# Performance work log

Measured on AMD Instinct MI355X. Metric: run time of the kernel, lower is better.

The kernel has to match this reference:

```python
import jax, jax.numpy as jnp
import numpy as np

B, S, E_DIM, H_DIM, WID, HGT = 64, 128, 256, 128, 64, 64


def setup_inputs() -> dict:
    key = jax.random.key(0)
    k1, k2, k3, k4 = jax.random.split(key, 4)
    e = jax.random.normal(k1, (B, S, E_DIM), dtype=jnp.float32)
    h = jax.random.normal(k2, (B, H_DIM, WID, HGT), dtype=jnp.float32)
    W = jax.random.normal(k3, (H_DIM, E_DIM), dtype=jnp.float32) * (1.0 / np.sqrt(E_DIM))
    b = jax.random.normal(k4, (H_DIM,), dtype=jnp.float32) * 0.01
    return {"e": e, "h": h, "W": W, "b": b}


def reference(e, h, W, b):
    # Linear: (B, S, e_dim) -> (B, S, h_dim)
    ep = jnp.einsum('bse,de->bsd', e, W) + b
    batch, ch, width, height = h.shape
    hv = h.reshape(batch, ch, width * height)          # (B, D, N)
    # scores s = bmm(e^T_proj, h): (B, S, N)
    s = jnp.einsum('bsd,bdn->bsn', ep, hv)
    # softmax over seq dim (dim=1 in torch)
    beta = jax.nn.softmax(s, axis=1)
    # c = sum_s e[b,d,s] * beta[b,s,n]  -> (B, D, N)  (true batched GEMM)
    c = jnp.einsum('bsd,bsn->bdn', ep, beta)
    return c.reshape(batch, ch, width, height)
```

## Files before the change

kernel.cpp:

```cpp
#include <hip/hip_runtime.h>
#include <math.h>

#define B_ 64
#define S_ 128
#define E_ 256
#define D_ 128
#define N_ 4096

typedef _Float16 f16;
typedef _Float16 f16x8 __attribute__((ext_vector_type(8)));
typedef float f32x4 __attribute__((ext_vector_type(4)));

__device__ __forceinline__ unsigned pack2(f16 a, f16 b) {
    union { f16 h[2]; unsigned u; } x;
    x.h[0] = a; x.h[1] = b; return x.u;
}

__device__ __forceinline__ f32x4 mfma16(f16x8 a, f16x8 b, f32x4 c) {
    return __builtin_amdgcn_mfma_f32_16x16x32_f16(a, b, c, 0, 0, 0);
}

__global__ __launch_bounds__(256) void k1_ep(
    const float* __restrict__ e, const float* __restrict__ W,
    const float* __restrict__ bias,
    unsigned* __restrict__ epA_h, unsigned* __restrict__ epA_l,
    unsigned* __restrict__ epT_h)
{
    __shared__ __align__(16) float el[64 * 68];
    __shared__ __align__(16) float Wl[32 * 68];
    const int t = threadIdx.x;
    const int b  = blockIdx.x >> 3;
    const int d0 = ((blockIdx.x >> 1) & 3) << 5;
    const int s0 = (blockIdx.x & 1) << 6;
    const int p = t & 15;
    const int q = t >> 4;

    float acc[2][2][2];
#pragma unroll
    for (int m = 0; m < 2; ++m)
#pragma unroll
        for (int u = 0; u < 2; ++u)
            acc[m][u][0] = acc[m][u][1] = 0.f;

    for (int kc = 0; kc < E_; kc += 64) {
#pragma unroll
        for (int it = 0; it < 4; ++it) {
            const int lin = it * 256 + t;
            const int r = lin >> 4, c4 = (lin & 15) << 2;
            *(float4*)(el + r * 68 + c4) =
                *(const float4*)(e + (b * S_ + s0 + r) * E_ + kc + c4);
        }
#pragma unroll
        for (int it = 0; it < 2; ++it) {
            const int lin = it * 256 + t;
            const int r = lin >> 4, c4 = (lin & 15) << 2;
            *(float4*)(Wl + r * 68 + c4) =
                *(const float4*)(W + (d0 + r) * E_ + kc + c4);
        }
        __syncthreads();
#pragma unroll 4
        for (int kk = 0; kk < 64; kk += 4) {
            const float4 w0 = *(const float4*)(Wl + (2 * p) * 68 + kk);
            const float4 w1 = *(const float4*)(Wl + (2 * p + 1) * 68 + kk);
#pragma unroll
            for (int u = 0; u < 2; ++u) {
                const float4 e0 = *(const float4*)(el + (2 * q + 32 * u) * 68 + kk);
                const float4 e1 = *(const float4*)(el + (2 * q + 1 + 32 * u) * 68 + kk);
                acc[0][u][0] += w0.x * e0.x + w0.y * e0.y + w0.z * e0.z + w0.w * e0.w;
                acc[0][u][1] += w0.x * e1.x + w0.y * e1.y + w0.z * e1.z + w0.w * e1.w;
                acc[1][u][0] += w1.x * e0.x + w1.y * e0.y + w1.z * e0.z + w1.w * e0.w;
                acc[1][u][1] += w1.x * e1.x + w1.y * e1.y + w1.z * e1.z + w1.w * e1.w;
            }
        }
        __syncthreads();
    }

    const float bz[2] = { bias[d0 + 2 * p], bias[d0 + 2 * p + 1] };
    f16 hi[2][2][2], lo[2][2][2];
#pragma unroll
    for (int m = 0; m < 2; ++m)
#pragma unroll
        for (int u = 0; u < 2; ++u)
#pragma unroll
            for (int v = 0; v < 2; ++v) {
                const float val = acc[m][u][v] + bz[m];
                const f16 h_ = (f16)val;
                hi[m][u][v] = h_;
                lo[m][u][v] = (f16)(val - (float)h_);
            }
#pragma unroll
    for (int u = 0; u < 2; ++u)
#pragma unroll
        for (int v = 0; v < 2; ++v) {
            const int s = s0 + 2 * q + v + 32 * u;
            const int w = (b * S_ + s) * 64 + (d0 >> 1) + p;
            epA_h[w] = pack2(hi[0][u][v], hi[1][u][v]);
            epA_l[w] = pack2(lo[0][u][v], lo[1][u][v]);
        }
#pragma unroll
    for (int m = 0; m < 2; ++m)
#pragma unroll
        for (int u = 0; u < 2; ++u) {
            const int d = d0 + 2 * p + m;
            const int w = (b * D_ + d) * 64 + (s0 >> 1) + q + 16 * u;
            epT_h[w] = pack2(hi[m][u][0], hi[m][u][1]);
        }
}

__global__ __launch_bounds__(256) void k2_attn(
    const float* __restrict__ h, const f16* __restrict__ epA_h,
    const f16* __restrict__ epA_l, const f16* __restrict__ epT_h,
    float* __restrict__ out)
{
    __shared__ __align__(16) unsigned char reg1[34816];
    __shared__ __align__(16) unsigned char reg2[17408];
    __shared__ float red1[4][64];
    __shared__ float red2[4][64];

    f16*   hT_h = (f16*)reg1;
    f16*   hT_l = (f16*)(reg1 + 17408);
    float* sc   = (float*)reg1;
    float* cb   = (float*)reg1;
    f16*   bT   = (f16*)reg2;
    float* stg  = (float*)reg2;

    const int t = threadIdx.x;
    const int b  = blockIdx.x >> 6;
    const int n0 = (blockIdx.x & 63) << 6;
    const int wid = t >> 6, lane = t & 63;
    const int l16 = lane & 15, quad = lane >> 4;

    const int jj = t & 63;
    const int dg = (t >> 6) << 3;
    unsigned* dstH = (unsigned*)hT_h;
    unsigned* dstL = (unsigned*)hT_l;
    for (int ch = 0; ch < 4; ++ch) {
#pragma unroll
        for (int r = 0; r < 2; ++r) {
            const int lin = r * 256 + t;
            const int dd = lin >> 4, m4 = (lin & 15) << 2;
            *(float4*)(stg + dd * 68 + m4) =
                *(const float4*)(h + (b * D_ + ch * 32 + dd) * N_ + n0 + m4);
        }
        __syncthreads();
        f16 vh[8], vl[8];
#pragma unroll
        for (int x = 0; x < 8; ++x) {
            const float v = stg[(dg + x) * 68 + jj];
            vh[x] = (f16)v;
            vl[x] = (f16)(v - (float)vh[x]);
        }
        const int base = jj * 68 + (ch << 4) + (dg >> 1);
#pragma unroll
        for (int y = 0; y < 4; ++y) {
            dstH[base + y] = pack2(vh[2 * y], vh[2 * y + 1]);
            dstL[base + y] = pack2(vl[2 * y], vl[2 * y + 1]);
        }
        __syncthreads();
    }

    const int sb = wid << 5;
    f32x4 acc[2][4];
#pragma unroll
    for (int mt = 0; mt < 2; ++mt)
#pragma unroll
        for (int nt = 0; nt < 4; ++nt) acc[mt][nt] = (f32x4)0.f;

    const f16* Ah = epA_h + (b * S_ + sb + l16) * D_ + quad * 8;
    const f16* Al = epA_l + (b * S_ + sb + l16) * D_ + quad * 8;
#pragma unroll
    for (int kk = 0; kk < 4; ++kk) {
        const int dc = kk << 5;
        f16x8 bh[4], bl[4];
#pragma unroll
        for (int nt = 0; nt < 4; ++nt) {
            const int idx = ((nt << 4) + l16) * 136 + dc + quad * 8;
            bh[nt] = *(const f16x8*)(hT_h + idx);
            bl[nt] = *(const f16x8*)(hT_l + idx);
        }
#pragma unroll
        for (int mt = 0; mt < 2; ++mt) {
            const f16x8 ah = *(const f16x8*)(Ah + mt * 16 * D_ + dc);
            const f16x8 al = *(const f16x8*)(Al + mt * 16 * D_ + dc);
#pragma unroll
            for (int nt = 0; nt < 4; ++nt) {
                acc[mt][nt] = mfma16(ah, bh[nt], acc[mt][nt]);
                acc[mt][nt] = mfma16(ah, bl[nt], acc[mt][nt]);
                acc[mt][nt] = mfma16(al, bh[nt], acc[mt][nt]);
            }
        }
    }
    __syncthreads();
#pragma unroll
    for (int mt = 0; mt < 2; ++mt)
#pragma unroll
        for (int nt = 0; nt < 4; ++nt)
#pragma unroll
            for (int r = 0; r < 4; ++r)
                sc[(sb + mt * 16 + quad * 4 + r) * 68 + (nt << 4) + l16] =
                    acc[mt][nt][r];
    __syncthreads();

    const int pj = t & 63, pp = t >> 6;
    float ev[32];
    float mx = -1e30f;
#pragma unroll
    for (int ss = 0; ss < 32; ++ss) {
        ev[ss] = sc[(pp * 32 + ss) * 68 + pj];
        mx = fmaxf(mx, ev[ss]);
    }
    red1[pp][pj] = mx;
    __syncthreads();
    mx = fmaxf(fmaxf(red1[0][pj], red1[1][pj]),
               fmaxf(red1[2][pj], red1[3][pj]));
    float sm = 0.f;
#pragma unroll
    for (int ss = 0; ss < 32; ++ss) {
        ev[ss] = expf(ev[ss] - mx);
        sm += ev[ss];
    }
    red2[pp][pj] = sm;
    __syncthreads();
    sm = red2[0][pj] + red2[1][pj] + red2[2][pj] + red2[3][pj];
    const float inv = 1.f / sm;
    unsigned* bTw = (unsigned*)bT;
    const int bbase = pj * 68 + pp * 16;
#pragma unroll
    for (int k = 0; k < 16; ++k)
        bTw[bbase + k] = pack2((f16)(ev[2 * k] * inv), (f16)(ev[2 * k + 1] * inv));
    __syncthreads();

    const int db = wid << 5;
    f32x4 a2[2][4];
#pragma unroll
    for (int mt = 0; mt < 2; ++mt)
#pragma unroll
        for (int nt = 0; nt < 4; ++nt) a2[mt][nt] = (f32x4)0.f;

    const f16* At = epT_h + (b * D_ + db + l16) * S_ + quad * 8;
#pragma unroll
    for (int kk = 0; kk < 4; ++kk) {
        const int scb = kk << 5;
        f16x8 bb[4];
#pragma unroll
        for (int nt = 0; nt < 4; ++nt)
            bb[nt] = *(const f16x8*)(bT + ((nt << 4) + l16) * 136 + scb + quad * 8);
#pragma unroll
        for (int mt = 0; mt < 2; ++mt) {
            const f16x8 av = *(const f16x8*)(At + mt * 16 * S_ + scb);
#pragma unroll
            for (int nt = 0; nt < 4; ++nt)
                a2[mt][nt] = mfma16(av, bb[nt], a2[mt][nt]);
        }
    }
#pragma unroll
    for (int mt = 0; mt < 2; ++mt)
#pragma unroll
        for (int nt = 0; nt < 4; ++nt)
#pragma unroll
            for (int r = 0; r < 4; ++r)
                cb[(db + mt * 16 + quad * 4 + r) * 68 + (nt << 4) + l16] =
                    a2[mt][nt][r];
    __syncthreads();

#pragma unroll
    for (int r = 0; r < 8; ++r) {
        const int lin = r * 256 + t;
        const int row = lin >> 4, c4 = (lin & 15) << 2;
        *(float4*)(out + (b * D_ + row) * N_ + n0 + c4) =
            *(float4*)(cb + row * 68 + c4);
    }
}

extern "C" void kernel_launch(void* const* d_in, const int* in_sizes, int n_in,
                              void* d_out, int out_size, void* d_ws, size_t ws_size,
                              hipStream_t stream) {
    const float* e    = (const float*)d_in[0];
    const float* h    = (const float*)d_in[1];
    const float* W    = (const float*)d_in[2];
    const float* bias = (const float*)d_in[3];
    float* out = (float*)d_out;

    unsigned* epA_h = (unsigned*)d_ws;
    unsigned* epA_l = epA_h + (B_ * S_ * D_ / 2);
    unsigned* epT_h = epA_l + (B_ * S_ * D_ / 2);

    hipLaunchKernelGGL(k1_ep, dim3(B_ * 8), dim3(256), 0, stream,
                       e, W, bias, epA_h, epA_l, epT_h);
    hipLaunchKernelGGL(k2_attn, dim3(B_ * 64), dim3(256), 0, stream,
                       h, (const f16*)epA_h, (const f16*)epA_l,
                       (const f16*)epT_h, out);
}
```

Baseline: 299.8 us.

## Halve N-tile to 32 columns, do softmax in registers, swizzle LDS, store output directly

The attention kernel now processes 32 spatial columns per block instead of 64, doubling the grid and shrinking LDS use so more blocks fit per CU. It loads the whole h tile in one pass and writes the hi/lo fp16 split into XOR-swizzled LDS. The softmax max and sum are computed on the MFMA accumulators with cross-lane shuffles plus a small LDS reduction, which removes the score round-trip through LDS. The output is written straight from registers. The epA operands are now re-read from global memory twice as often, and the direct output stores are narrower and less coalesced than the previous float4 staging.

```diff
diff --git a/kernel.cpp b/kernel.cpp
--- a/kernel.cpp
+++ b/kernel.cpp
@@ -112,164 +112,173 @@
     const f16* __restrict__ epA_l, const f16* __restrict__ epT_h,
     float* __restrict__ out)
 {
-    __shared__ __align__(16) unsigned char reg1[34816];
-    __shared__ __align__(16) unsigned char reg2[17408];
-    __shared__ float red1[4][64];
-    __shared__ float red2[4][64];
-
-    f16*   hT_h = (f16*)reg1;
-    f16*   hT_l = (f16*)(reg1 + 17408);
-    float* sc   = (float*)reg1;
-    float* cb   = (float*)reg1;
-    f16*   bT   = (f16*)reg2;
-    float* stg  = (float*)reg2;
+    __shared__ __align__(16) unsigned char regA[16384];
+    __shared__ __align__(16) unsigned char regB[18432];
+
+    f16*   hTh  = (f16*)regA;
+    f16*   hTl  = (f16*)(regA + 8192);
+    float* stg  = (float*)regB;
+    f16*   bT   = (f16*)regB;
+    float* red1 = (float*)(regB + 8704);
+    float* red2 = (float*)(regB + 9216);
 
     const int t = threadIdx.x;
-    const int b  = blockIdx.x >> 6;
-    const int n0 = (blockIdx.x & 63) << 6;
+    const int b  = blockIdx.x >> 7;
+    const int n0 = (blockIdx.x & 127) << 5;
     const int wid = t >> 6, lane = t & 63;
     const int l16 = lane & 15, quad = lane >> 4;
 
-    const int jj = t & 63;
-    const int dg = (t >> 6) << 3;
-    unsigned* dstH = (unsigned*)hT_h;
-    unsigned* dstL = (unsigned*)hT_l;
-    for (int ch = 0; ch < 4; ++ch) {
-#pragma unroll
-        for (int r = 0; r < 2; ++r) {
-            const int lin = r * 256 + t;
-            const int dd = lin >> 4, m4 = (lin & 15) << 2;
-            *(float4*)(stg + dd * 68 + m4) =
-                *(const float4*)(h + (b * D_ + ch * 32 + dd) * N_ + n0 + m4);
-        }
-        __syncthreads();
-        f16 vh[8], vl[8];
-#pragma unroll
-        for (int x = 0; x < 8; ++x) {
-            const float v = stg[(dg + x) * 68 + jj];
-            vh[x] = (f16)v;
-            vl[x] = (f16)(v - (float)vh[x]);
-        }
-        const int base = jj * 68 + (ch << 4) + (dg >> 1);
-#pragma unroll
-        for (int y = 0; y < 4; ++y) {
-            dstH[base + y] = pack2(vh[2 * y], vh[2 * y + 1]);
-            dstL[base + y] = pack2(vl[2 * y], vl[2 * y + 1]);
-        }
-        __syncthreads();
-    }
+    float4 v[4];
+#pragma unroll
+    for (int i = 0; i < 4; ++i) {
+        const int lin = i * 256 + t;
+        const int d = lin >> 3, c4 = (lin & 7) << 2;
+        v[i] = *(const float4*)(h + (b * D_ + d) * N_ + n0 + c4);
+    }
+#pragma unroll
+    for (int i = 0; i < 4; ++i) {
+        const int lin = i * 256 + t;
+        const int d = lin >> 3, c4 = (lin & 7) << 2;
+        *(float4*)(stg + d * 36 + c4) = v[i];
+    }
+    __syncthreads();
+
+    {
+        const int n = t & 31, dgrp = t >> 5;
+        f16x8 h0, h1, l0, l1;
+#pragma unroll
+        for (int x = 0; x < 16; ++x) {
+            const float val = stg[(dgrp * 16 + x) * 36 + n];
+            const f16 hi_ = (f16)val;
+            const f16 lo_ = (f16)(val - (float)hi_);
+            if (x < 8) { h0[x] = hi_; l0[x] = lo_; }
+            else       { h1[x - 8] = hi_; l1[x - 8] = lo_; }
+        }
+        const int base = n * 256 + dgrp * 32;
+        const int swz  = (n & 7) << 4;
+        *(f16x8*)((char*)hTh + ((base)      ^ swz)) = h0;
+        *(f16x8*)((char*)hTh + ((base + 16) ^ swz)) = h1;
+        *(f16x8*)((char*)hTl + ((base)      ^ swz)) = l0;
+        *(f16x8*)((char*)hTl + ((base + 16) ^ swz)) = l1;
+    }
+    __syncthreads();
 
     const int sb = wid << 5;
-    f32x4 acc[2][4];
+    f32x4 acc[2][2];
 #pragma unroll
     for (int mt = 0; mt < 2; ++mt)
 #pragma unroll
-        for (int nt = 0; nt < 4; ++nt) acc[mt][nt] = (f32x4)0.f;
+        for (int nt = 0; nt < 2; ++nt) acc[mt][nt] = (f32x4)0.f;
 
     const f16* Ah = epA_h + (b * S_ + sb + l16) * D_ + quad * 8;
     const f16* Al = epA_l + (b * S_ + sb + l16) * D_ + quad * 8;
 #pragma unroll
     for (int kk = 0; kk < 4; ++kk) {
         const int dc = kk << 5;
-        f16x8 bh[4], bl[4];
-#pragma unroll
-        for (int nt = 0; nt < 4; ++nt) {
-            const int idx = ((nt << 4) + l16) * 136 + dc + quad * 8;
-            bh[nt] = *(const f16x8*)(hT_h + idx);
-            bl[nt] = *(const f16x8*)(hT_l + idx);
+        f16x8 bh[2], bl[2];
+#pragma unroll
+        for (int nt = 0; nt < 2; ++nt) {
+            const int n = (nt << 4) + l16;
+            const int off = (n * 256 + dc * 2 + quad * 16) ^ ((n & 7) << 4);
+            bh[nt] = *(const f16x8*)((const char*)hTh + off);
+            bl[nt] = *(const f16x8*)((const char*)hTl + off);
         }
 #pragma unroll
         for (int mt = 0; mt < 2; ++mt) {
             const f16x8 ah = *(const f16x8*)(Ah + mt * 16 * D_ + dc);
             const f16x8 al = *(const f16x8*)(Al + mt * 16 * D_ + dc);
 #pragma unroll
-            for (int nt = 0; nt < 4; ++nt) {
+            for (int nt = 0; nt < 2; ++nt) {
                 acc[mt][nt] = mfma16(ah, bh[nt], acc[mt][nt]);
                 acc[mt][nt] = mfma16(ah, bl[nt], acc[mt][nt]);
                 acc[mt][nt] = mfma16(al, bh[nt], acc[mt][nt]);
             }
         }
     }
-    __syncthreads();
+
+#pragma unroll
+    for (int nt = 0; nt < 2; ++nt) {
+        float pm = -1e30f;
+#pragma unroll
+        for (int mt = 0; mt < 2; ++mt)
+#pragma unroll
+            for (int r = 0; r < 4; ++r) pm = fmaxf(pm, acc[mt][nt][r]);
+        pm = fmaxf(pm, __shfl_xor(pm, 16));
+        pm = fmaxf(pm, __shfl_xor(pm, 32));
+        if (quad == 0) red1[(((nt << 4) + l16) << 2) + wid] = pm;
+    }
+    __syncthreads();
+
+    float ev[2][2][4];
+#pragma unroll
+    for (int nt = 0; nt < 2; ++nt) {
+        const f32x4 m4 = *(const f32x4*)(red1 + (((nt << 4) + l16) << 2));
+        const float mx = fmaxf(fmaxf(m4[0], m4[1]), fmaxf(m4[2], m4[3]));
+        float ps = 0.f;
+#pragma unroll
+        for (int mt = 0; mt < 2; ++mt)
+#pragma unroll
+            for (int r = 0; r < 4; ++r) {
+                const float e_ = __expf(acc[mt][nt][r] - mx);
+                ev[mt][nt][r] = e_;
+                ps += e_;
+            }
+        ps += __shfl_xor(ps, 16);
+        ps += __shfl_xor(ps, 32);
+        if (quad == 0) red2[(((nt << 4) + l16) << 2) + wid] = ps;
+    }
+    __syncthreads();
+
+    unsigned* bTw = (unsigned*)bT;
+#pragma unroll
+    for (int nt = 0; nt < 2; ++nt) {
+        const int n = (nt << 4) + l16;
+        const f32x4 s4 = *(const f32x4*)(red2 + (n << 2));
+        const float inv = 1.f / (s4[0] + s4[1] + s4[2] + s4[3]);
+#pragma unroll
+        for (int mt = 0; mt < 2; ++mt) {
+            const int wbase = n * 68 + ((sb + mt * 16) >> 1) + quad * 2;
+            bTw[wbase]     = pack2((f16)(ev[mt][nt][0] * inv),
+                                   (f16)(ev[mt][nt][1] * inv));
+            bTw[wbase + 1] = pack2((f16)(ev[mt][nt][2] * inv),
+                                   (f16)(ev[mt][nt][3] * inv));
+        }
+    }
+    __syncthreads();
+
+    const int db = wid << 5;
+    f32x4 a2[2][2];
 #pragma unroll
     for (int mt = 0; mt < 2; ++mt)
 #pragma unroll
-        for (int nt = 0; nt < 4; ++nt)
-#pragma unroll
-            for (int r = 0; r < 4; ++r)
-                sc[(sb + mt * 16 + quad * 4 + r) * 68 + (nt << 4) + l16] =
-                    acc[mt][nt][r];
-    __syncthreads();
-
-    const int pj = t & 63, pp = t >> 6;
-    float ev[32];
-    float mx = -1e30f;
-#pragma unroll
-    for (int ss = 0; ss < 32; ++ss) {
-        ev[ss] = sc[(pp * 32 + ss) * 68 + pj];
-        mx = fmaxf(mx, ev[ss]);
-    }
-    red1[pp][pj] = mx;
-    __syncthreads();
-    mx = fmaxf(fmaxf(red1[0][pj], red1[1][pj]),
-               fmaxf(red1[2][pj], red1[3][pj]));
-    float sm = 0.f;
-#pragma unroll
-    for (int ss = 0; ss < 32; ++ss) {
-        ev[ss] = expf(ev[ss] - mx);
-        sm += ev[ss];
-    }
-    red2[pp][pj] = sm;
-    __syncthreads();
-    sm = red2[0][pj] + red2[1][pj] + red2[2][pj] + red2[3][pj];
-    const float inv = 1.f / sm;
-    unsigned* bTw = (unsigned*)bT;
-    const int bbase = pj * 68 + pp * 16;
-#pragma unroll
-    for (int k = 0; k < 16; ++k)
-        bTw[bbase + k] = pack2((f16)(ev[2 * k] * inv), (f16)(ev[2 * k + 1] * inv));
-    __syncthreads();
-
-    const int db = wid << 5;
-    f32x4 a2[2][4];
-#pragma unroll
-    for (int mt = 0; mt < 2; ++mt)
-#pragma unroll
-        for (int nt = 0; nt < 4; ++nt) a2[mt][nt] = (f32x4)0.f;
+        for (int nt = 0; nt < 2; ++nt) a2[mt][nt] = (f32x4)0.f;
 
     const f16* At = epT_h + (b * D_ + db + l16) * S_ + quad * 8;
 #pragma unroll
     for (int kk = 0; kk < 4; ++kk) {
         const int scb = kk << 5;
-        f16x8 bb[4];
-#pragma unroll
-        for (int nt = 0; nt < 4; ++nt)
+        f16x8 bb[2];
+#pragma unroll
+        for (int nt = 0; nt < 2; ++nt)
             bb[nt] = *(const f16x8*)(bT + ((nt << 4) + l16) * 136 + scb + quad * 8);
 #pragma unroll
         for (int mt = 0; mt < 2; ++mt) {
             const f16x8 av = *(const f16x8*)(At + mt * 16 * S_ + scb);
 #pragma unroll
-            for (int nt = 0; nt < 4; ++nt)
+            for (int nt = 0; nt < 2; ++nt)
                 a2[mt][nt] = mfma16(av, bb[nt], a2[mt][nt]);
         }
     }
+
+    float* ob = out + (b * D_ + db) * N_ + n0;
 #pragma unroll
     for (int mt = 0; mt < 2; ++mt)
 #pragma unroll
-        for (int nt = 0; nt < 4; ++nt)
+        for (int nt = 0; nt < 2; ++nt)
 #pragma unroll
             for (int r = 0; r < 4; ++r)
-                cb[(db + mt * 16 + quad * 4 + r) * 68 + (nt << 4) + l16] =
+                ob[(mt * 16 + quad * 4 + r) * N_ + (nt << 4) + l16] =
                     a2[mt][nt][r];
-    __syncthreads();
-
-#pragma unroll
-    for (int r = 0; r < 8; ++r) {
-        const int lin = r * 256 + t;
-        const int row = lin >> 4, c4 = (lin & 15) << 2;
-        *(float4*)(out + (b * D_ + row) * N_ + n0 + c4) =
-            *(float4*)(cb + row * 68 + c4);
-    }
 }
 
 extern "C" void kernel_launch(void* const* d_in, const int* in_sizes, int n_in,
@@ -287,7 +296,7 @@
 
     hipLaunchKernelGGL(k1_ep, dim3(B_ * 8), dim3(256), 0, stream,
                        e, W, bias, epA_h, epA_l, epT_h);
-    hipLaunchKernelGGL(k2_attn, dim3(B_ * 64), dim3(256), 0, stream,
+    hipLaunchKernelGGL(k2_attn, dim3(B_ * 128), dim3(256), 0, stream,
                        h, (const f16*)epA_h, (const f16*)epA_l,
                        (const f16*)epT_h, out);
 }
```

After: 317.9 us. 6.0% more time.
